# Kernel tuning notes

Measured on AMD Instinct MI355X. Metric: run time of the kernel, lower is better.

The kernel has to match this reference:

```python
import jax, jax.numpy as jnp
import numpy as np


def setup_inputs() -> dict:
    key = jax.random.key(0)
    ks = jax.random.split(key, 4)
    L, B, T, H, D = 12, 4, 2048, 16, 64
    current_layer = jax.random.normal(ks[0], (B, T, H, D), dtype=jnp.float32)
    all_layers = jax.random.normal(ks[1], (L, B, T, H, D), dtype=jnp.float32)
    # nn.init.normal_(std=0.02) for both projections
    Wq = jax.random.normal(ks[2], (D, D), dtype=jnp.float32) * 0.02
    Wk = jax.random.normal(ks[3], (D, D), dtype=jnp.float32) * 0.02
    scales = jnp.full((L,), 1.0 / L, dtype=jnp.float32)  # LayerScalingFactor init 1/num_layers
    temperature = jnp.ones((1,), dtype=jnp.float32)
    return {
        "current_layer": current_layer,
        "all_layers": all_layers,
        "Wq": Wq,
        "Wk": Wk,
        "scales": scales,
        "temperature": temperature,
        "current_layer_idx": 0,
    }


def reference(current_layer, all_layers, Wq, Wk, scales, temperature, current_layer_idx):
    # current_layer: [B,T,H,D]; all_layers: [L,B,T,H,D] (stack of per-layer outputs)
    # num_heads = 1, so per-head dim == D and scores are over the layer axis L.
    D = current_layer.shape[-1]
    q = jnp.einsum("bthd,ed->bthe", current_layer, Wq)          # query_proj (no bias)
    k = jnp.einsum("lbthd,ed->lbthe", all_layers, Wk)           # key_proj (no bias)
    inv_scale = 1.0 / (jnp.sqrt(jnp.asarray(D, q.dtype)) * jnp.abs(temperature[0]))
    scores = jnp.einsum("bthd,lbthd->bthl", q, k) * inv_scale   # [B,T,H,L]
    attn = jax.nn.softmax(scores, axis=-1)
    attn = attn * scales                                        # per-layer learned scale
    attn = attn / (jnp.sum(attn, axis=-1, keepdims=True) + 1e-6)  # renormalize
    # per-layer accumulation: output += scales[l] * attn[...,l] * all_layers[l]
    out = jnp.einsum("bthl,l,lbthd->bthd", attn, scales, all_layers)
    return out
```

## Files before the change

### kernel.cpp

```cpp
#include <hip/hip_runtime.h>

constexpr int L = 12;
constexpr int B = 4, T = 2048, H = 16, D = 64;
constexpr int NPOS = B * T * H;
constexpr long long SLAYER = (long long)NPOS * D;
constexpr int P = 16;

__global__ __launch_bounds__(64) void cla_precompute_Mt(
    const float* __restrict__ Wq, const float* __restrict__ Wk,
    float* __restrict__ Mt) {
  const int d = blockIdx.x;
  const int c = threadIdx.x;
  float acc = 0.f;
  #pragma unroll
  for (int e = 0; e < D; ++e)
    acc = fmaf(Wq[e * D + d], Wk[e * D + c], acc);
  Mt[c * D + d] = acc;
}

template <int CTRL, int ROWM>
__device__ __forceinline__ float dpp_add(float x) {
  int moved = __builtin_amdgcn_update_dpp(0, __float_as_int(x), CTRL, ROWM, 0xF,
                                          false);
  return x + __int_as_float(moved);
}

__device__ __forceinline__ float wave_sum_bcast(float x) {
  x = dpp_add<0x111, 0xF>(x);
  x = dpp_add<0x112, 0xF>(x);
  x = dpp_add<0x114, 0xF>(x);
  x = dpp_add<0x118, 0xF>(x);
  x = dpp_add<0x142, 0xA>(x);
  x = dpp_add<0x143, 0xC>(x);
  return __int_as_float(__builtin_amdgcn_readlane(__float_as_int(x), 63));
}

__global__ __launch_bounds__(256) void cla_main(
    const float* __restrict__ cur, const float* __restrict__ all,
    const float* __restrict__ Mt, const float* __restrict__ scales,
    const float* __restrict__ temperature, float* __restrict__ out) {
  const int lane = threadIdx.x & 63;
  const int wloc = __builtin_amdgcn_readfirstlane(threadIdx.x >> 6);
  const int wid  = blockIdx.x * 4 + wloc;

  float Mc[D];
  {
    const float4* mt = (const float4*)(Mt + lane * D);
    #pragma unroll
    for (int c = 0; c < 16; ++c) {
      const float4 m = mt[c];
      Mc[4 * c + 0] = m.x;
      Mc[4 * c + 1] = m.y;
      Mc[4 * c + 2] = m.z;
      Mc[4 * c + 3] = m.w;
    }
  }

  const float inv_scale = 1.0f / (8.0f * fabsf(temperature[0]));
  float scl[L];
  #pragma unroll
  for (int l = 0; l < L; ++l) scl[l] = scales[l];

  const int pos0 = wid * P;
  for (int it = 0; it < P; ++it) {
    const int pos = pos0 + it;
    const size_t pbase = (size_t)pos * D;

    const float4* xp = (const float4*)(cur + pbase);
    float v = 0.f;
    #pragma unroll
    for (int dc = 0; dc < 4; ++dc) {
      const float4 a = xp[4 * dc + 0];
      const float4 b = xp[4 * dc + 1];
      const float4 c = xp[4 * dc + 2];
      const float4 d = xp[4 * dc + 3];
      v = fmaf(a.x, Mc[16 * dc + 0], v);
      v = fmaf(a.y, Mc[16 * dc + 1], v);
      v = fmaf(a.z, Mc[16 * dc + 2], v);
      v = fmaf(a.w, Mc[16 * dc + 3], v);
      v = fmaf(b.x, Mc[16 * dc + 4], v);
      v = fmaf(b.y, Mc[16 * dc + 5], v);
      v = fmaf(b.z, Mc[16 * dc + 6], v);
      v = fmaf(b.w, Mc[16 * dc + 7], v);
      v = fmaf(c.x, Mc[16 * dc + 8], v);
      v = fmaf(c.y, Mc[16 * dc + 9], v);
      v = fmaf(c.z, Mc[16 * dc + 10], v);
      v = fmaf(c.w, Mc[16 * dc + 11], v);
      v = fmaf(d.x, Mc[16 * dc + 12], v);
      v = fmaf(d.y, Mc[16 * dc + 13], v);
      v = fmaf(d.z, Mc[16 * dc + 14], v);
      v = fmaf(d.w, Mc[16 * dc + 15], v);
    }

    float yv[L];
    #pragma unroll
    for (int l = 0; l < L; ++l)
      yv[l] = all[(size_t)l * SLAYER + pbase + lane];

    float sc[L];
    #pragma unroll
    for (int l = 0; l < L; ++l)
      sc[l] = wave_sum_bcast(v * yv[l]) * inv_scale;

    float mx = sc[0];
    #pragma unroll
    for (int l = 1; l < L; ++l) mx = fmaxf(mx, sc[l]);
    float sum = 0.f;
    #pragma unroll
    for (int l = 0; l < L; ++l) { sc[l] = __expf(sc[l] - mx); sum += sc[l]; }
    const float inv_sum = 1.0f / sum;

    float w[L];
    float ssum = 0.f;
    #pragma unroll
    for (int l = 0; l < L; ++l) {
      w[l] = sc[l] * inv_sum * scl[l];
      ssum += w[l];
    }
    const float r = 1.0f / (ssum + 1e-6f);

    float o = 0.f;
    #pragma unroll
    for (int l = 0; l < L; ++l) o = fmaf(w[l] * r * scl[l], yv[l], o);
    out[pbase + lane] = o;
  }
}

extern "C" void kernel_launch(void* const* d_in, const int* in_sizes, int n_in,
                              void* d_out, int out_size, void* d_ws, size_t ws_size,
                              hipStream_t stream) {
  const float* cur    = (const float*)d_in[0];
  const float* all    = (const float*)d_in[1];
  const float* Wq     = (const float*)d_in[2];
  const float* Wk     = (const float*)d_in[3];
  const float* scales = (const float*)d_in[4];
  const float* temp   = (const float*)d_in[5];
  float* Mt = (float*)d_ws;

  cla_precompute_Mt<<<64, 64, 0, stream>>>(Wq, Wk, Mt);

  const int nwaves  = NPOS / P;
  const int nblocks = nwaves / 4;
  cla_main<<<nblocks, 256, 0, stream>>>(cur, all, Mt, scales, temp,
                                        (float*)d_out);
}
```

Before: 121.4 us.

## Process four positions per wave with float4 loads and 16-lane row reductions

Each wave now handles four positions at once. Every lane loads a float4 of each layer's row, and the score reduction becomes a 16-lane DPP row rotate sum instead of a full-wave reduction with a readlane broadcast. The projected query values pass through LDS so each 16-lane group gets its position's q vector, and outputs are written as float4. This cuts the reduction instruction count and the number of memory transactions per byte, at the cost of more registers (12 float4 values live) and an LDS round trip.

```diff
diff --git a/kernel.cpp b/kernel.cpp
--- a/kernel.cpp
+++ b/kernel.cpp
@@ -4,7 +4,7 @@
 constexpr int B = 4, T = 2048, H = 16, D = 64;
 constexpr int NPOS = B * T * H;
 constexpr long long SLAYER = (long long)NPOS * D;
-constexpr int P = 16;
+constexpr int PITER = 4;
 
 __global__ __launch_bounds__(64) void cla_precompute_Mt(
     const float* __restrict__ Wq, const float* __restrict__ Wk,
@@ -18,30 +18,29 @@
   Mt[c * D + d] = acc;
 }
 
-template <int CTRL, int ROWM>
-__device__ __forceinline__ float dpp_add(float x) {
-  int moved = __builtin_amdgcn_update_dpp(0, __float_as_int(x), CTRL, ROWM, 0xF,
+template <int CTRL>
+__device__ __forceinline__ float ror_add(float x) {
+  int moved = __builtin_amdgcn_update_dpp(0, __float_as_int(x), CTRL, 0xF, 0xF,
                                           false);
   return x + __int_as_float(moved);
 }
-
-__device__ __forceinline__ float wave_sum_bcast(float x) {
-  x = dpp_add<0x111, 0xF>(x);
-  x = dpp_add<0x112, 0xF>(x);
-  x = dpp_add<0x114, 0xF>(x);
-  x = dpp_add<0x118, 0xF>(x);
-  x = dpp_add<0x142, 0xA>(x);
-  x = dpp_add<0x143, 0xC>(x);
-  return __int_as_float(__builtin_amdgcn_readlane(__float_as_int(x), 63));
+__device__ __forceinline__ float row_sum16(float x) {
+  x = ror_add<0x121>(x);
+  x = ror_add<0x122>(x);
+  x = ror_add<0x124>(x);
+  x = ror_add<0x128>(x);
+  return x;
 }
 
 __global__ __launch_bounds__(256) void cla_main(
     const float* __restrict__ cur, const float* __restrict__ all,
     const float* __restrict__ Mt, const float* __restrict__ scales,
     const float* __restrict__ temperature, float* __restrict__ out) {
+  __shared__ float vlds[4][4 * D];
+
   const int lane = threadIdx.x & 63;
-  const int wloc = __builtin_amdgcn_readfirstlane(threadIdx.x >> 6);
-  const int wid  = blockIdx.x * 4 + wloc;
+  const int w    = __builtin_amdgcn_readfirstlane(threadIdx.x >> 6);
+  const int wid  = blockIdx.x * 4 + w;
 
   float Mc[D];
   {
@@ -61,46 +60,41 @@
   #pragma unroll
   for (int l = 0; l < L; ++l) scl[l] = scales[l];
 
-  const int pos0 = wid * P;
-  for (int it = 0; it < P; ++it) {
-    const int pos = pos0 + it;
-    const size_t pbase = (size_t)pos * D;
+  const int g = lane >> 4;
+  const int j = lane & 15;
 
-    const float4* xp = (const float4*)(cur + pbase);
-    float v = 0.f;
+  for (int t = 0; t < PITER; ++t) {
+    const int pos0 = (wid * PITER + t) * 4;
+    const size_t base = (size_t)pos0 * D;
+
     #pragma unroll
-    for (int dc = 0; dc < 4; ++dc) {
-      const float4 a = xp[4 * dc + 0];
-      const float4 b = xp[4 * dc + 1];
-      const float4 c = xp[4 * dc + 2];
-      const float4 d = xp[4 * dc + 3];
-      v = fmaf(a.x, Mc[16 * dc + 0], v);
-      v = fmaf(a.y, Mc[16 * dc + 1], v);
-      v = fmaf(a.z, Mc[16 * dc + 2], v);
-      v = fmaf(a.w, Mc[16 * dc + 3], v);
-      v = fmaf(b.x, Mc[16 * dc + 4], v);
-      v = fmaf(b.y, Mc[16 * dc + 5], v);
-      v = fmaf(b.z, Mc[16 * dc + 6], v);
-      v = fmaf(b.w, Mc[16 * dc + 7], v);
-      v = fmaf(c.x, Mc[16 * dc + 8], v);
-      v = fmaf(c.y, Mc[16 * dc + 9], v);
-      v = fmaf(c.z, Mc[16 * dc + 10], v);
-      v = fmaf(c.w, Mc[16 * dc + 11], v);
-      v = fmaf(d.x, Mc[16 * dc + 12], v);
-      v = fmaf(d.y, Mc[16 * dc + 13], v);
-      v = fmaf(d.z, Mc[16 * dc + 14], v);
-      v = fmaf(d.w, Mc[16 * dc + 15], v);
+    for (int p = 0; p < 4; ++p) {
+      const float4* xp = (const float4*)(cur + base + (size_t)p * D);
+      float v = 0.f;
+      #pragma unroll
+      for (int c4 = 0; c4 < 16; ++c4) {
+        const float4 xv = xp[c4];
+        v = fmaf(xv.x, Mc[4 * c4 + 0], v);
+        v = fmaf(xv.y, Mc[4 * c4 + 1], v);
+        v = fmaf(xv.z, Mc[4 * c4 + 2], v);
+        v = fmaf(xv.w, Mc[4 * c4 + 3], v);
+      }
+      vlds[w][p * D + lane] = v;
     }
 
-    float yv[L];
+    const float4 q = *(const float4*)&vlds[w][g * D + 4 * j];
+
+    float4 y[L];
     #pragma unroll
     for (int l = 0; l < L; ++l)
-      yv[l] = all[(size_t)l * SLAYER + pbase + lane];
+      y[l] = ((const float4*)(all + (size_t)l * SLAYER + base))[lane];
 
     float sc[L];
     #pragma unroll
-    for (int l = 0; l < L; ++l)
-      sc[l] = wave_sum_bcast(v * yv[l]) * inv_scale;
+    for (int l = 0; l < L; ++l) {
+      float s = q.x * y[l].x + q.y * y[l].y + q.z * y[l].z + q.w * y[l].w;
+      sc[l] = row_sum16(s) * inv_scale;
+    }
 
     float mx = sc[0];
     #pragma unroll
@@ -110,19 +104,25 @@
     for (int l = 0; l < L; ++l) { sc[l] = __expf(sc[l] - mx); sum += sc[l]; }
     const float inv_sum = 1.0f / sum;
 
-    float w[L];
+    float wgt[L];
     float ssum = 0.f;
     #pragma unroll
     for (int l = 0; l < L; ++l) {
-      w[l] = sc[l] * inv_sum * scl[l];
-      ssum += w[l];
+      wgt[l] = sc[l] * inv_sum * scl[l];
+      ssum += wgt[l];
     }
     const float r = 1.0f / (ssum + 1e-6f);
 
-    float o = 0.f;
+    float o0 = 0.f, o1 = 0.f, o2 = 0.f, o3 = 0.f;
     #pragma unroll
-    for (int l = 0; l < L; ++l) o = fmaf(w[l] * r * scl[l], yv[l], o);
-    out[pbase + lane] = o;
+    for (int l = 0; l < L; ++l) {
+      const float wl = wgt[l] * r * scl[l];
+      o0 = fmaf(wl, y[l].x, o0);
+      o1 = fmaf(wl, y[l].y, o1);
+      o2 = fmaf(wl, y[l].z, o2);
+      o3 = fmaf(wl, y[l].w, o3);
+    }
+    ((float4*)(out + base))[lane] = make_float4(o0, o1, o2, o3);
   }
 }
 
@@ -139,8 +139,7 @@
 
   cla_precompute_Mt<<<64, 64, 0, stream>>>(Wq, Wk, Mt);
 
-  const int nwaves  = NPOS / P;
-  const int nblocks = nwaves / 4;
+  const int nblocks = NPOS / (4 * PITER * 4);
   cla_main<<<nblocks, 256, 0, stream>>>(cur, all, Mt, scales, temp,
                                         (float*)d_out);
 }
```

New measurement: 158.3 us. 30.3% more time.
